# Kernel optimization log

Measured on AMD Instinct MI355X. Metric: run time of the kernel, lower is better.

## Reference

```python
import jax, jax.numpy as jnp
import numpy as np

N_NODES = 646  # fixed by nn.LayerNorm([646, 64])
LN_EPS = 1e-5


def gcn_conv(x, edge_index, W, b):
    """PyG GCNConv: out = D^-1/2 (A+I) D^-1/2 (x W) + b, scatter-add at target."""
    n = x.shape[0]
    h = x @ W  # [N, out_dim]
    loop = jnp.arange(n, dtype=edge_index.dtype)
    row = jnp.concatenate([edge_index[0], loop])  # source
    col = jnp.concatenate([edge_index[1], loop])  # target
    deg = jax.ops.segment_sum(jnp.ones_like(col, dtype=h.dtype), col, num_segments=n)
    dinv = jnp.where(deg > 0, jax.lax.rsqrt(deg), 0.0)
    norm = dinv[row] * dinv[col]  # [E+N]
    out = jax.ops.segment_sum(h[row] * norm[:, None], col, num_segments=n)
    return out + b


def setup_inputs() -> dict:
    key = jax.random.key(0)
    ks = jax.random.split(key, 8)
    F, H, L, E = 32768, 64, 128, 646 * 64
    x = jax.random.normal(ks[0], (N_NODES, F), dtype=jnp.float32)
    edge_index = jax.random.randint(ks[1], (2, E), 0, N_NODES, dtype=jnp.int64)
    s = 1.0 / np.sqrt(F)
    W1 = jax.random.normal(ks[2], (F, H), dtype=jnp.float32) * s
    b1 = jax.random.normal(ks[3], (H,), dtype=jnp.float32) * 0.01
    W2 = jax.random.normal(ks[4], (H, L), dtype=jnp.float32) * (1.0 / np.sqrt(H))
    b2 = jax.random.normal(ks[5], (L,), dtype=jnp.float32) * 0.01
    LPw = jax.random.normal(ks[6], (F, H), dtype=jnp.float32) * s
    LPb = jax.random.normal(ks[7], (H,), dtype=jnp.float32) * 0.01
    return {"x": x, "edge_index": edge_index, "W1": W1, "b1": b1,
            "W2": W2, "b2": b2, "LPw": LPw, "LPb": LPb}


def reference(x, edge_index, W1, b1, W2, b2, LPw, LPb):
    res = x @ LPw + LPb                       # Linear residual branch [N, 64]
    h = gcn_conv(x, edge_index, W1, b1)       # GCN1 [N, 64]
    h = res + h
    h = h * jax.nn.sigmoid(h)                 # SiLU
    # LayerNorm over BOTH dims [646, 64], no affine (elementwise_affine=False)
    mu = jnp.mean(h)
    var = jnp.mean(jnp.square(h - mu))
    h = (h - mu) * jax.lax.rsqrt(var + LN_EPS)
    out = gcn_conv(h, edge_index, W2, b2)     # GCN2 [N, num_label]
    return out
```

## Files before the change

kernel.cpp:

```cpp
#include <hip/hip_runtime.h>
#include <hip/hip_bf16.h>

#define NN 646
#define FF 32768
#define HH 64
#define LL 128
#define TOT (NN*HH)
#define OUTTOT (NN*LL)
#define WT_STRIDE (FF + 32)
#define KSPLIT 64
#define KSLICE (FF / KSPLIT)
#define BK 32
#define NSTEP (KSLICE / BK)
#define NMT 6
#define NGEMM (NMT * KSPLIT)

typedef float f32x4 __attribute__((ext_vector_type(4)));
typedef short short8 __attribute__((ext_vector_type(8)));

__device__ __forceinline__ unsigned short f2bf(float f) {
  __hip_bfloat16 h = __float2bfloat16(f);
  return __builtin_bit_cast(unsigned short, h);
}
__device__ __forceinline__ short8 pack8(float4 u, float4 v) {
  short8 r;
  r[0] = (short)f2bf(u.x); r[1] = (short)f2bf(u.y);
  r[2] = (short)f2bf(u.z); r[3] = (short)f2bf(u.w);
  r[4] = (short)f2bf(v.x); r[5] = (short)f2bf(v.y);
  r[6] = (short)f2bf(v.z); r[7] = (short)f2bf(v.w);
  return r;
}
__device__ __forceinline__ void gload16(const void* g, void* l) {
  __builtin_amdgcn_global_load_lds(
      (const __attribute__((address_space(1))) void*)g,
      (__attribute__((address_space(3))) void*)l, 16, 0, 0);
}
__device__ __forceinline__ bool probe_i64(const int* e32, int* orr) {
  if (threadIdx.x == 0) *orr = 0;
  __syncthreads();
  if (threadIdx.x < 256 && e32[2 * threadIdx.x + 1] != 0) atomicOr(orr, 1);
  __syncthreads();
  return *orr == 0;
}

__global__ __launch_bounds__(1024) void k_zero(int* __restrict__ cnt,
                                               float* __restrict__ stats) {
  int t = threadIdx.x;
  if (t < NN) cnt[t] = 0;
  if (t < 2) stats[t] = 0.f;
}

__global__ __launch_bounds__(256) void k_init(const float* __restrict__ W1,
                                              const float* __restrict__ LPw,
                                              unsigned short* __restrict__ wt,
                                              const int* __restrict__ e32, int E,
                                              int* __restrict__ cnt,
                                              const float* __restrict__ W2,
                                              float* __restrict__ cs) {
  if (blockIdx.x < 512) {
    __shared__ float t[64][129];
    int k0 = blockIdx.x * 64;
    for (int idx = threadIdx.x; idx < 64 * 128; idx += 256) {
      int kk = idx >> 7, n = idx & 127;
      float v = (n < 64) ? W1[(size_t)(k0 + kk) * 64 + n]
                         : LPw[(size_t)(k0 + kk) * 64 + (n - 64)];
      t[kk][n] = v;
    }
    __syncthreads();
    for (int idx = threadIdx.x; idx < 1024; idx += 256) {
      int n = idx >> 3;
      int kc = (idx & 7) * 8;
      short8 v;
#pragma unroll
      for (int u = 0; u < 8; ++u) v[u] = (short)f2bf(t[kc + u][n]);
      *reinterpret_cast<short8*>(&wt[(size_t)n * WT_STRIDE + k0 + kc]) = v;
    }
    return;
  }
  if (blockIdx.x == 576) {
    __shared__ float r2[2][128];
    int j = threadIdx.x & 127, h = threadIdx.x >> 7;
    float a = 0.f;
    for (int k = h * 32; k < h * 32 + 32; ++k) a += W2[k * LL + j];
    r2[h][j] = a;
    __syncthreads();
    if (h == 0) cs[j] = r2[0][j] + r2[1][j];
    return;
  }
  __shared__ int orr;
  bool i64 = probe_i64(e32, &orr);
  const int* cp = i64 ? (e32 + 2 * (size_t)E) : (e32 + E);
  int st = i64 ? 2 : 1;
  int wid = (blockIdx.x - 512) * 256 + threadIdx.x;
  for (int e = wid; e < E; e += 64 * 256)
    atomicAdd(&cnt[cp[(size_t)e * st]], 1);
}

__global__ __launch_bounds__(256, 3) void k_gemm(const float* __restrict__ x,
                                                 const unsigned short* __restrict__ wt,
                                                 float* __restrict__ partial,
                                                 const int* __restrict__ cnt, int E,
                                                 int* __restrict__ offsets,
                                                 float* __restrict__ dinv,
                                                 int* __restrict__ cursor) {
  __shared__ __align__(16) float As[2][128 * BK];
  __shared__ __align__(16) unsigned short Bs[2][128 * BK];

  int p = blockIdx.x;
  if (p == NGEMM) {
    __shared__ int wtot[4];
    int tid = threadIdx.x;
    int b = 3 * tid;
    int c0 = (b < NN) ? cnt[b] : 0;
    int c1 = (b + 1 < NN) ? cnt[b + 1] : 0;
    int c2 = (b + 2 < NN) ? cnt[b + 2] : 0;
    int s = c0 + c1 + c2;
    int lane = tid & 63, wv = tid >> 6;
    int run = s;
#pragma unroll
    for (int o = 1; o < 64; o <<= 1) { int v = __shfl_up(run, o); if (lane >= o) run += v; }
    if (lane == 63) wtot[wv] = run;
    __syncthreads();
    int wbase = 0;
    for (int i = 0; i < wv; ++i) wbase += wtot[i];
    int excl = wbase + run - s;
    if (b < NN)     { offsets[b]     = excl;           cursor[b]     = excl;           dinv[b]     = rsqrtf((float)(c0 + 1)); }
    if (b + 1 < NN) { offsets[b + 1] = excl + c0;      cursor[b + 1] = excl + c0;      dinv[b + 1] = rsqrtf((float)(c1 + 1)); }
    if (b + 2 < NN) { offsets[b + 2] = excl + c0 + c1; cursor[b + 2] = excl + c0 + c1; dinv[b + 2] = rsqrtf((float)(c2 + 1)); }
    if (tid == 0) offsets[NN] = E;
    return;
  }

  int xcd = p & 7, idx = p >> 3;
  int ks = xcd + 8 * (idx / NMT);
  int mt = idx % NMT;
  int tid = threadIdx.x;
  int w = tid >> 6, l = tid & 63;
  int lr = l & 15, g = l >> 4;
  int wr = w * 32;
  int ksbase = ks * KSLICE;

  f32x4 acc[2][8];
#pragma unroll
  for (int i = 0; i < 2; ++i)
#pragma unroll
    for (int j = 0; j < 8; ++j) acc[i][j] = (f32x4){0.f, 0.f, 0.f, 0.f};

  auto STAGE = [&](int buf, int step) {
    int kb = ksbase + step * BK;
#pragma unroll
    for (int j = 0; j < 4; ++j) {
      int pp = j * 256 + tid;
      int row = pp >> 3, cc = pp & 7;
      int c = cc ^ (row & 7);
      int rowg = mt * 128 + row; if (rowg > NN - 1) rowg = NN - 1;
      gload16(x + (size_t)rowg * FF + kb + c * 4, (char*)(&As[buf][0]) + pp * 16);
    }
#pragma unroll
    for (int j = 0; j < 2; ++j) {
      int pp = j * 256 + tid;
      int row = pp >> 2, cc = pp & 3;
      int c = cc ^ (row & 3);
      gload16(wt + (size_t)row * WT_STRIDE + kb + c * 8,
              (char*)(&Bs[buf][0]) + pp * 16);
    }
  };

  auto COMPUTE = [&](int buf) {
    const char* Ab = (const char*)(&As[buf][0]);
    const char* Bb = (const char*)(&Bs[buf][0]);
    short8 af0, af1;
    {
      int row = wr + lr, rm = row & 7;
      float4 lo = *(const float4*)(Ab + (row * 8 + ((g * 2) ^ rm)) * 16);
      float4 hi = *(const float4*)(Ab + (row * 8 + ((g * 2 + 1) ^ rm)) * 16);
      af0 = pack8(lo, hi);
    }
    {
      int row = wr + 16 + lr, rm = row & 7;
      float4 lo = *(const float4*)(Ab + (row * 8 + ((g * 2) ^ rm)) * 16);
      float4 hi = *(const float4*)(Ab + (row * 8 + ((g * 2 + 1) ^ rm)) * 16);
      af1 = pack8(lo, hi);
    }
#pragma unroll
    for (int nf = 0; nf < 8; ++nf) {
      int brow = nf * 16 + lr;
      short8 b = *(const short8*)(Bb + (brow * 4 + (g ^ (brow & 3))) * 16);
      acc[0][nf] = __builtin_amdgcn_mfma_f32_16x16x32_bf16(af0, b, acc[0][nf], 0, 0, 0);
      acc[1][nf] = __builtin_amdgcn_mfma_f32_16x16x32_bf16(af1, b, acc[1][nf], 0, 0, 0);
    }
  };

  STAGE(0, 0);
  STAGE(1, 1);
#pragma unroll
  for (int t = 0; t < NSTEP; ++t) {
    if (t + 1 < NSTEP) {
      asm volatile("s_waitcnt vmcnt(6)" ::: "memory");
    } else {
      asm volatile("s_waitcnt vmcnt(0)" ::: "memory");
    }
    __builtin_amdgcn_s_barrier();
    COMPUTE(t & 1);
    if (t + 2 < NSTEP) {
      __builtin_amdgcn_s_barrier();
      STAGE(t & 1, t + 2);
    }
  }

  float* pp = partial + (size_t)ks * OUTTOT;
#pragma unroll
  for (int mf = 0; mf < 2; ++mf) {
#pragma unroll
    for (int nf = 0; nf < 8; ++nf) {
#pragma unroll
      for (int j = 0; j < 4; ++j) {
        int m = mt * 128 + wr + mf * 16 + g * 4 + j;
        if (m < NN) pp[m * LL + nf * 16 + lr] = acc[mf][nf][j];
      }
    }
  }
}

__global__ __launch_bounds__(256) void k_redplace(const float* __restrict__ partial,
                                                  const float* __restrict__ LPb,
                                                  float* __restrict__ hcat,
                                                  const int* __restrict__ e32, int E,
                                                  int* __restrict__ cursor,
                                                  int* __restrict__ srcs) {
  if (blockIdx.x < 81) {
    int i4 = blockIdx.x * 256 + threadIdx.x;
    if (i4 * 4 >= OUTTOT) return;
    f32x4 s = {0.f, 0.f, 0.f, 0.f};
#pragma unroll 8
    for (int ks = 0; ks < KSPLIT; ++ks)
      s += *reinterpret_cast<const f32x4*>(partial + (size_t)ks * OUTTOT + i4 * 4);
    int n = (i4 * 4) & 127;
    if (n & 64) s += *reinterpret_cast<const f32x4*>(LPb + (n - 64));
    *reinterpret_cast<f32x4*>(hcat + i4 * 4) = s;
    return;
  }
  __shared__ int orr;
  bool i64 = probe_i64(e32, &orr);
  int e = (blockIdx.x - 81) * 256 + threadIdx.x;
  if (e >= E) return;
  const int* rp = e32;
  const int* cp = i64 ? (e32 + 2 * (size_t)E) : (e32 + E);
  int st = i64 ? 2 : 1;
  int r = rp[(size_t)e * st];
  int c = cp[(size_t)e * st];
  int pos = atomicAdd(&cursor[c], 1);
  srcs[pos] = r;
}

__global__ __launch_bounds__(256) void k_fuse1(const int* __restrict__ offs,
                                               const int* __restrict__ srcs,
                                               const float* __restrict__ dinv,
                                               const float* __restrict__ hcat,
                                               const float* __restrict__ b1,
                                               const float* __restrict__ W2,
                                               float* __restrict__ hwr,
                                               float* __restrict__ sdi,
                                               float* __restrict__ stats) {
  int c = blockIdx.x;
  int j = threadIdx.x & 63, qt = threadIdx.x >> 6;
  int o0 = offs[c], o1 = offs[c + 1];
  float acc = 0.f, sd = 0.f;
  for (int i = o0 + qt; i < o1; i += 4) {
    int r = srcs[i];
    float dr = dinv[r];
    acc += hcat[r * LL + j] * dr;
    sd += dr;
  }
  __shared__ float red[4][64];
  __shared__ float sdl[4];
  __shared__ float hnl[64];
  red[qt][j] = acc;
  if (j == 0) sdl[qt] = sd;
  __syncthreads();
  if (qt == 0) {
    float di = dinv[c];
    float gb = (red[0][j] + red[1][j] + red[2][j] + red[3][j]) * di;
    float t = hcat[c * LL + 64 + j] + b1[j] + gb + hcat[c * LL + j] * di * di;
    float s = t / (1.f + __expf(-t));
    hnl[j] = s;
    float sum = s, sq = s * s;
#pragma unroll
    for (int o = 32; o; o >>= 1) { sum += __shfl_down(sum, o); sq += __shfl_down(sq, o); }
    if (j == 0) {
      atomicAdd(&stats[0], sum);
      atomicAdd(&stats[1], sq);
      sdi[c] = sdl[0] + sdl[1] + sdl[2] + sdl[3] + di;
    }
  }
  __syncthreads();
  int j2 = threadIdx.x & 127, h = threadIdx.x >> 7;
  float a2 = 0.f;
#pragma unroll
  for (int k = h * 32; k < h * 32 + 32; ++k) a2 += hnl[k] * W2[k * LL + j2];
  __shared__ float r2[2][128];
  r2[h][j2] = a2;
  __syncthreads();
  if (h == 0) hwr[c * LL + j2] = (r2[0][j2] + r2[1][j2]) * dinv[c];
}

__global__ __launch_bounds__(256) void k_fuse2(const int* __restrict__ offs,
                                               const int* __restrict__ srcs,
                                               const float* __restrict__ dinv,
                                               const float* __restrict__ hwr,
                                               const float* __restrict__ b2,
                                               const float* __restrict__ cs,
                                               const float* __restrict__ sdi,
                                               const float* __restrict__ stats,
                                               float* __restrict__ out) {
  int c = blockIdx.x;
  int j = threadIdx.x & 127, hf = threadIdx.x >> 7;
  int o0 = offs[c], o1 = offs[c + 1];
  float acc = 0.f;
  for (int i = o0 + hf; i < o1; i += 2) acc += hwr[srcs[i] * LL + j];
  __shared__ float red[2][128];
  red[hf][j] = acc;
  __syncthreads();
  if (hf == 0) {
    float mu = stats[0] * (1.f / TOT);
    float var = stats[1] * (1.f / TOT) - mu * mu;
    float rs = rsqrtf(var + 1e-5f);
    float S = red[0][j] + red[1][j] + hwr[c * LL + j];
    out[c * LL + j] = b2[j] + dinv[c] * (rs * S - rs * mu * cs[j] * sdi[c]);
  }
}

extern "C" void kernel_launch(void* const* d_in, const int* in_sizes, int n_in,
                              void* d_out, int out_size, void* d_ws, size_t ws_size,
                              hipStream_t stream) {
  const float* x   = (const float*)d_in[0];
  const int*   e32 = (const int*)d_in[1];
  const float* W1  = (const float*)d_in[2];
  const float* b1  = (const float*)d_in[3];
  const float* W2  = (const float*)d_in[4];
  const float* b2  = (const float*)d_in[5];
  const float* LPw = (const float*)d_in[6];
  const float* LPb = (const float*)d_in[7];
  int E = in_sizes[1] / 2;
  float* out = (float*)d_out;

  char* ws = (char*)d_ws;
  size_t o_wt      = 0;
  size_t o_partial = 8396800;
  size_t o_hcat    = o_partial + (size_t)KSPLIT * OUTTOT * 4;
  size_t o_hwr     = o_hcat + 330752;
  size_t o_dinv    = o_hwr + 330752;
  size_t o_offs    = o_dinv + 2816;
  size_t o_cnt     = o_offs + 2816;
  size_t o_stat    = o_cnt + 2816;
  size_t o_cur     = o_stat + 256;
  size_t o_srcs    = o_cur + 2816;
  size_t o_cs      = o_srcs + 165376;
  size_t o_sdi     = o_cs + 512;

  unsigned short* wt = (unsigned short*)(ws + o_wt);
  float* partial = (float*)(ws + o_partial);
  float* hcat    = (float*)(ws + o_hcat);
  float* hwr     = (float*)(ws + o_hwr);
  float* dinv    = (float*)(ws + o_dinv);
  int*   offs    = (int*)(ws + o_offs);
  int*   cnt     = (int*)(ws + o_cnt);
  float* stats   = (float*)(ws + o_stat);
  int*   cursor  = (int*)(ws + o_cur);
  int*   srcs    = (int*)(ws + o_srcs);
  float* cs      = (float*)(ws + o_cs);
  float* sdi     = (float*)(ws + o_sdi);

  k_zero<<<1, 1024, 0, stream>>>(cnt, stats);
  k_init<<<577, 256, 0, stream>>>(W1, LPw, wt, e32, E, cnt, W2, cs);
  k_gemm<<<NGEMM + 1, 256, 0, stream>>>(x, wt, partial, cnt, E, offs, dinv, cursor);
  k_redplace<<<243, 256, 0, stream>>>(partial, LPb, hcat, e32, E, cursor, srcs);
  k_fuse1<<<NN, 256, 0, stream>>>(offs, srcs, dinv, hcat, b1, W2, hwr, sdi, stats);
  k_fuse2<<<NN, 256, 0, stream>>>(offs, srcs, dinv, hwr, b2, cs, sdi, stats, out);
}
```

Measured before the change: 94.20 us.

## Replace split-K partial buffer and reduction with atomic accumulation into hcat

The split-K GEMM now atomically adds its 64 partial tiles straight into hcat instead of writing a 64-slice partial buffer that a separate kernel summed. hcat is pre-filled with the LPb bias in a new pre-kernel that also zeroes the counters. The standalone edge-placement kernel keeps only the CSR scatter. This removes about 21 MB of partial writes and reads plus one reduction pass, at the cost of 64-way float atomic contention per output element and a summation order that is no longer deterministic.

```diff
diff --git a/kernel.cpp b/kernel.cpp
--- a/kernel.cpp
+++ b/kernel.cpp
@@ -43,10 +43,22 @@
   return *orr == 0;
 }
 
-__global__ __launch_bounds__(1024) void k_zero(int* __restrict__ cnt,
-                                               float* __restrict__ stats) {
+__global__ __launch_bounds__(256) void k_pre(const float* __restrict__ LPb,
+                                             float* __restrict__ hcat,
+                                             int* __restrict__ cnt,
+                                             float* __restrict__ stats) {
+  if (blockIdx.x < 81) {
+    int i4 = blockIdx.x * 256 + threadIdx.x;
+    if (i4 * 4 < OUTTOT) {
+      int n = (i4 * 4) & 127;
+      f32x4 v = {0.f, 0.f, 0.f, 0.f};
+      if (n & 64) v = *reinterpret_cast<const f32x4*>(LPb + (n - 64));
+      *reinterpret_cast<f32x4*>(hcat + i4 * 4) = v;
+    }
+    return;
+  }
   int t = threadIdx.x;
-  if (t < NN) cnt[t] = 0;
+  for (int i = t; i < 648; i += 256) cnt[i] = 0;
   if (t < 2) stats[t] = 0.f;
 }
 
@@ -98,7 +110,7 @@
 
 __global__ __launch_bounds__(256, 3) void k_gemm(const float* __restrict__ x,
                                                  const unsigned short* __restrict__ wt,
-                                                 float* __restrict__ partial,
+                                                 float* __restrict__ hcat,
                                                  const int* __restrict__ cnt, int E,
                                                  int* __restrict__ offsets,
                                                  float* __restrict__ dinv,
@@ -140,11 +152,9 @@
   int wr = w * 32;
   int ksbase = ks * KSLICE;
 
-  f32x4 acc[2][8];
-#pragma unroll
-  for (int i = 0; i < 2; ++i)
-#pragma unroll
-    for (int j = 0; j < 8; ++j) acc[i][j] = (f32x4){0.f, 0.f, 0.f, 0.f};
+  f32x4 z = {0.f, 0.f, 0.f, 0.f};
+  f32x4 a00 = z, a01 = z, a02 = z, a03 = z, a04 = z, a05 = z, a06 = z, a07 = z;
+  f32x4 a10 = z, a11 = z, a12 = z, a13 = z, a14 = z, a15 = z, a16 = z, a17 = z;
 
   auto STAGE = [&](int buf, int step) {
     int kb = ksbase + step * BK;
@@ -182,13 +192,16 @@
       float4 hi = *(const float4*)(Ab + (row * 8 + ((g * 2 + 1) ^ rm)) * 16);
       af1 = pack8(lo, hi);
     }
-#pragma unroll
-    for (int nf = 0; nf < 8; ++nf) {
-      int brow = nf * 16 + lr;
-      short8 b = *(const short8*)(Bb + (brow * 4 + (g ^ (brow & 3))) * 16);
-      acc[0][nf] = __builtin_amdgcn_mfma_f32_16x16x32_bf16(af0, b, acc[0][nf], 0, 0, 0);
-      acc[1][nf] = __builtin_amdgcn_mfma_f32_16x16x32_bf16(af1, b, acc[1][nf], 0, 0, 0);
-    }
+#define DO_NF(NF, A0, A1)                                                        \
+    {                                                                            \
+      int brow = NF * 16 + lr;                                                   \
+      short8 bv = *(const short8*)(Bb + (brow * 4 + (g ^ (brow & 3))) * 16);     \
+      A0 = __builtin_amdgcn_mfma_f32_16x16x32_bf16(af0, bv, A0, 0, 0, 0);        \
+      A1 = __builtin_amdgcn_mfma_f32_16x16x32_bf16(af1, bv, A1, 0, 0, 0);        \
+    }
+    DO_NF(0, a00, a10) DO_NF(1, a01, a11) DO_NF(2, a02, a12) DO_NF(3, a03, a13)
+    DO_NF(4, a04, a14) DO_NF(5, a05, a15) DO_NF(6, a06, a16) DO_NF(7, a07, a17)
+#undef DO_NF
   };
 
   STAGE(0, 0);
@@ -208,41 +221,27 @@
     }
   }
 
-  float* pp = partial + (size_t)ks * OUTTOT;
-#pragma unroll
-  for (int mf = 0; mf < 2; ++mf) {
-#pragma unroll
-    for (int nf = 0; nf < 8; ++nf) {
-#pragma unroll
-      for (int j = 0; j < 4; ++j) {
-        int m = mt * 128 + wr + mf * 16 + g * 4 + j;
-        if (m < NN) pp[m * LL + nf * 16 + lr] = acc[mf][nf][j];
-      }
-    }
-  }
-}
-
-__global__ __launch_bounds__(256) void k_redplace(const float* __restrict__ partial,
-                                                  const float* __restrict__ LPb,
-                                                  float* __restrict__ hcat,
-                                                  const int* __restrict__ e32, int E,
-                                                  int* __restrict__ cursor,
-                                                  int* __restrict__ srcs) {
-  if (blockIdx.x < 81) {
-    int i4 = blockIdx.x * 256 + threadIdx.x;
-    if (i4 * 4 >= OUTTOT) return;
-    f32x4 s = {0.f, 0.f, 0.f, 0.f};
-#pragma unroll 8
-    for (int ks = 0; ks < KSPLIT; ++ks)
-      s += *reinterpret_cast<const f32x4*>(partial + (size_t)ks * OUTTOT + i4 * 4);
-    int n = (i4 * 4) & 127;
-    if (n & 64) s += *reinterpret_cast<const f32x4*>(LPb + (n - 64));
-    *reinterpret_cast<f32x4*>(hcat + i4 * 4) = s;
-    return;
-  }
+#define EPI(MF, NF, ACC)                                                         \
+  {                                                                              \
+    _Pragma("unroll")                                                            \
+    for (int j = 0; j < 4; ++j) {                                                \
+      int m = mt * 128 + wr + MF * 16 + g * 4 + j;                               \
+      if (m < NN) atomicAdd(&hcat[m * LL + NF * 16 + lr], ACC[j]);               \
+    }                                                                            \
+  }
+  EPI(0, 0, a00) EPI(0, 1, a01) EPI(0, 2, a02) EPI(0, 3, a03)
+  EPI(0, 4, a04) EPI(0, 5, a05) EPI(0, 6, a06) EPI(0, 7, a07)
+  EPI(1, 0, a10) EPI(1, 1, a11) EPI(1, 2, a12) EPI(1, 3, a13)
+  EPI(1, 4, a14) EPI(1, 5, a15) EPI(1, 6, a16) EPI(1, 7, a17)
+#undef EPI
+}
+
+__global__ __launch_bounds__(256) void k_place(const int* __restrict__ e32, int E,
+                                               int* __restrict__ cursor,
+                                               int* __restrict__ srcs) {
   __shared__ int orr;
   bool i64 = probe_i64(e32, &orr);
-  int e = (blockIdx.x - 81) * 256 + threadIdx.x;
+  int e = blockIdx.x * 256 + threadIdx.x;
   if (e >= E) return;
   const int* rp = e32;
   const int* cp = i64 ? (e32 + 2 * (size_t)E) : (e32 + E);
@@ -345,36 +344,34 @@
   float* out = (float*)d_out;
 
   char* ws = (char*)d_ws;
-  size_t o_wt      = 0;
-  size_t o_partial = 8396800;
-  size_t o_hcat    = o_partial + (size_t)KSPLIT * OUTTOT * 4;
-  size_t o_hwr     = o_hcat + 330752;
-  size_t o_dinv    = o_hwr + 330752;
-  size_t o_offs    = o_dinv + 2816;
-  size_t o_cnt     = o_offs + 2816;
-  size_t o_stat    = o_cnt + 2816;
-  size_t o_cur     = o_stat + 256;
-  size_t o_srcs    = o_cur + 2816;
-  size_t o_cs      = o_srcs + 165376;
-  size_t o_sdi     = o_cs + 512;
+  size_t o_wt   = 0;
+  size_t o_hcat = 8396800;
+  size_t o_hwr  = o_hcat + 330752;
+  size_t o_dinv = o_hwr + 330752;
+  size_t o_offs = o_dinv + 2816;
+  size_t o_cnt  = o_offs + 2816;
+  size_t o_stat = o_cnt + 2816;
+  size_t o_cur  = o_stat + 256;
+  size_t o_srcs = o_cur + 2816;
+  size_t o_cs   = o_srcs + 165376;
+  size_t o_sdi  = o_cs + 512;
 
   unsigned short* wt = (unsigned short*)(ws + o_wt);
-  float* partial = (float*)(ws + o_partial);
-  float* hcat    = (float*)(ws + o_hcat);
-  float* hwr     = (float*)(ws + o_hwr);
-  float* dinv    = (float*)(ws + o_dinv);
-  int*   offs    = (int*)(ws + o_offs);
-  int*   cnt     = (int*)(ws + o_cnt);
-  float* stats   = (float*)(ws + o_stat);
-  int*   cursor  = (int*)(ws + o_cur);
-  int*   srcs    = (int*)(ws + o_srcs);
-  float* cs      = (float*)(ws + o_cs);
-  float* sdi     = (float*)(ws + o_sdi);
-
-  k_zero<<<1, 1024, 0, stream>>>(cnt, stats);
+  float* hcat   = (float*)(ws + o_hcat);
+  float* hwr    = (float*)(ws + o_hwr);
+  float* dinv   = (float*)(ws + o_dinv);
+  int*   offs   = (int*)(ws + o_offs);
+  int*   cnt    = (int*)(ws + o_cnt);
+  float* stats  = (float*)(ws + o_stat);
+  int*   cursor = (int*)(ws + o_cur);
+  int*   srcs   = (int*)(ws + o_srcs);
+  float* cs     = (float*)(ws + o_cs);
+  float* sdi    = (float*)(ws + o_sdi);
+
+  k_pre<<<82, 256, 0, stream>>>(LPb, hcat, cnt, stats);
   k_init<<<577, 256, 0, stream>>>(W1, LPw, wt, e32, E, cnt, W2, cs);
-  k_gemm<<<NGEMM + 1, 256, 0, stream>>>(x, wt, partial, cnt, E, offs, dinv, cursor);
-  k_redplace<<<243, 256, 0, stream>>>(partial, LPb, hcat, e32, E, cursor, srcs);
+  k_gemm<<<NGEMM + 1, 256, 0, stream>>>(x, wt, hcat, cnt, E, offs, dinv, cursor);
+  k_place<<<(E + 255) / 256, 256, 0, stream>>>(e32, E, cursor, srcs);
   k_fuse1<<<NN, 256, 0, stream>>>(offs, srcs, dinv, hcat, b1, W2, hwr, sdi, stats);
   k_fuse2<<<NN, 256, 0, stream>>>(offs, srcs, dinv, hwr, b2, cs, sdi, stats, out);
 }
```

Measured after the change: 109.3 us. 16.0% more time.

## Triple-buffer GEMM staging, per-block LDS histograms, drop zeroing kernel

Applied to the files above, without the earlier changes.

The GEMM main loop moves from double to triple LDS buffering. The next-next stage is issued before the current compute, so each step needs one barrier instead of two. This costs more shared memory and lowers the occupancy bound from 3 to 2 blocks per CU. Degree counting now uses per-block LDS histograms written to a partials array, which the scan block reduces. That removes the global atomics and the separate k_zero launch, with stats zeroed inside k_init. Accumulators are unrolled into named variables to keep them in registers.

```diff
diff --git a/kernel.cpp b/kernel.cpp
--- a/kernel.cpp
+++ b/kernel.cpp
@@ -43,20 +43,14 @@
   return *orr == 0;
 }
 
-__global__ __launch_bounds__(1024) void k_zero(int* __restrict__ cnt,
-                                               float* __restrict__ stats) {
-  int t = threadIdx.x;
-  if (t < NN) cnt[t] = 0;
-  if (t < 2) stats[t] = 0.f;
-}
-
 __global__ __launch_bounds__(256) void k_init(const float* __restrict__ W1,
                                               const float* __restrict__ LPw,
                                               unsigned short* __restrict__ wt,
                                               const int* __restrict__ e32, int E,
-                                              int* __restrict__ cnt,
+                                              int* __restrict__ cntp,
                                               const float* __restrict__ W2,
-                                              float* __restrict__ cs) {
+                                              float* __restrict__ cs,
+                                              float* __restrict__ stats) {
   if (blockIdx.x < 512) {
     __shared__ float t[64][129];
     int k0 = blockIdx.x * 64;
@@ -80,6 +74,7 @@
   if (blockIdx.x == 576) {
     __shared__ float r2[2][128];
     int j = threadIdx.x & 127, h = threadIdx.x >> 7;
+    if (threadIdx.x < 2) stats[threadIdx.x] = 0.f;
     float a = 0.f;
     for (int k = h * 32; k < h * 32 + 32; ++k) a += W2[k * LL + j];
     r2[h][j] = a;
@@ -87,33 +82,43 @@
     if (h == 0) cs[j] = r2[0][j] + r2[1][j];
     return;
   }
+  __shared__ int lcnt[648];
   __shared__ int orr;
+  int hb = blockIdx.x - 512;
+  for (int i = threadIdx.x; i < 648; i += 256) lcnt[i] = 0;
   bool i64 = probe_i64(e32, &orr);
   const int* cp = i64 ? (e32 + 2 * (size_t)E) : (e32 + E);
   int st = i64 ? 2 : 1;
-  int wid = (blockIdx.x - 512) * 256 + threadIdx.x;
-  for (int e = wid; e < E; e += 64 * 256)
-    atomicAdd(&cnt[cp[(size_t)e * st]], 1);
-}
-
-__global__ __launch_bounds__(256, 3) void k_gemm(const float* __restrict__ x,
+  for (int e = hb * 256 + threadIdx.x; e < E; e += 64 * 256)
+    atomicAdd(&lcnt[cp[(size_t)e * st]], 1);
+  __syncthreads();
+  for (int i = threadIdx.x; i < 648; i += 256) cntp[hb * 648 + i] = lcnt[i];
+}
+
+__global__ __launch_bounds__(256, 2) void k_gemm(const float* __restrict__ x,
                                                  const unsigned short* __restrict__ wt,
                                                  float* __restrict__ partial,
-                                                 const int* __restrict__ cnt, int E,
+                                                 const int* __restrict__ cntp, int E,
                                                  int* __restrict__ offsets,
                                                  float* __restrict__ dinv,
                                                  int* __restrict__ cursor) {
-  __shared__ __align__(16) float As[2][128 * BK];
-  __shared__ __align__(16) unsigned short Bs[2][128 * BK];
+  __shared__ __align__(16) float As[3][128 * BK];
+  __shared__ __align__(16) unsigned short Bs[3][128 * BK];
 
   int p = blockIdx.x;
   if (p == NGEMM) {
     __shared__ int wtot[4];
     int tid = threadIdx.x;
     int b = 3 * tid;
-    int c0 = (b < NN) ? cnt[b] : 0;
-    int c1 = (b + 1 < NN) ? cnt[b + 1] : 0;
-    int c2 = (b + 2 < NN) ? cnt[b + 2] : 0;
+    int c0 = 0, c1 = 0, c2 = 0;
+    if (b < NN) {
+#pragma unroll 8
+      for (int h = 0; h < 64; ++h) {
+        c0 += cntp[h * 648 + b];
+        c1 += (b + 1 < NN) ? cntp[h * 648 + b + 1] : 0;
+        c2 += (b + 2 < NN) ? cntp[h * 648 + b + 2] : 0;
+      }
+    }
     int s = c0 + c1 + c2;
     int lane = tid & 63, wv = tid >> 6;
     int run = s;
@@ -140,11 +145,9 @@
   int wr = w * 32;
   int ksbase = ks * KSLICE;
 
-  f32x4 acc[2][8];
-#pragma unroll
-  for (int i = 0; i < 2; ++i)
-#pragma unroll
-    for (int j = 0; j < 8; ++j) acc[i][j] = (f32x4){0.f, 0.f, 0.f, 0.f};
+  f32x4 z = {0.f, 0.f, 0.f, 0.f};
+  f32x4 a00 = z, a01 = z, a02 = z, a03 = z, a04 = z, a05 = z, a06 = z, a07 = z;
+  f32x4 a10 = z, a11 = z, a12 = z, a13 = z, a14 = z, a15 = z, a16 = z, a17 = z;
 
   auto STAGE = [&](int buf, int step) {
     int kb = ksbase + step * BK;
@@ -182,13 +185,16 @@
       float4 hi = *(const float4*)(Ab + (row * 8 + ((g * 2 + 1) ^ rm)) * 16);
       af1 = pack8(lo, hi);
     }
-#pragma unroll
-    for (int nf = 0; nf < 8; ++nf) {
-      int brow = nf * 16 + lr;
-      short8 b = *(const short8*)(Bb + (brow * 4 + (g ^ (brow & 3))) * 16);
-      acc[0][nf] = __builtin_amdgcn_mfma_f32_16x16x32_bf16(af0, b, acc[0][nf], 0, 0, 0);
-      acc[1][nf] = __builtin_amdgcn_mfma_f32_16x16x32_bf16(af1, b, acc[1][nf], 0, 0, 0);
-    }
+#define DO_NF(NF, A0, A1)                                                        \
+    {                                                                            \
+      int brow = NF * 16 + lr;                                                   \
+      short8 bv = *(const short8*)(Bb + (brow * 4 + (g ^ (brow & 3))) * 16);     \
+      A0 = __builtin_amdgcn_mfma_f32_16x16x32_bf16(af0, bv, A0, 0, 0, 0);        \
+      A1 = __builtin_amdgcn_mfma_f32_16x16x32_bf16(af1, bv, A1, 0, 0, 0);        \
+    }
+    DO_NF(0, a00, a10) DO_NF(1, a01, a11) DO_NF(2, a02, a12) DO_NF(3, a03, a13)
+    DO_NF(4, a04, a14) DO_NF(5, a05, a15) DO_NF(6, a06, a16) DO_NF(7, a07, a17)
+#undef DO_NF
   };
 
   STAGE(0, 0);
@@ -201,25 +207,24 @@
       asm volatile("s_waitcnt vmcnt(0)" ::: "memory");
     }
     __builtin_amdgcn_s_barrier();
-    COMPUTE(t & 1);
-    if (t + 2 < NSTEP) {
-      __builtin_amdgcn_s_barrier();
-      STAGE(t & 1, t + 2);
-    }
+    if (t + 2 < NSTEP) STAGE((t + 2) % 3, t + 2);
+    COMPUTE(t % 3);
   }
 
   float* pp = partial + (size_t)ks * OUTTOT;
-#pragma unroll
-  for (int mf = 0; mf < 2; ++mf) {
-#pragma unroll
-    for (int nf = 0; nf < 8; ++nf) {
-#pragma unroll
-      for (int j = 0; j < 4; ++j) {
-        int m = mt * 128 + wr + mf * 16 + g * 4 + j;
-        if (m < NN) pp[m * LL + nf * 16 + lr] = acc[mf][nf][j];
-      }
-    }
-  }
+#define EPI(MF, NF, ACC)                                                         \
+  {                                                                              \
+    _Pragma("unroll")                                                            \
+    for (int j = 0; j < 4; ++j) {                                                \
+      int m = mt * 128 + wr + MF * 16 + g * 4 + j;                               \
+      if (m < NN) pp[m * LL + NF * 16 + lr] = ACC[j];                            \
+    }                                                                            \
+  }
+  EPI(0, 0, a00) EPI(0, 1, a01) EPI(0, 2, a02) EPI(0, 3, a03)
+  EPI(0, 4, a04) EPI(0, 5, a05) EPI(0, 6, a06) EPI(0, 7, a07)
+  EPI(1, 0, a10) EPI(1, 1, a11) EPI(1, 2, a12) EPI(1, 3, a13)
+  EPI(1, 4, a14) EPI(1, 5, a15) EPI(1, 6, a16) EPI(1, 7, a17)
+#undef EPI
 }
 
 __global__ __launch_bounds__(256) void k_redplace(const float* __restrict__ partial,
@@ -351,8 +356,8 @@
   size_t o_hwr     = o_hcat + 330752;
   size_t o_dinv    = o_hwr + 330752;
   size_t o_offs    = o_dinv + 2816;
-  size_t o_cnt     = o_offs + 2816;
-  size_t o_stat    = o_cnt + 2816;
+  size_t o_cntp    = o_offs + 2816;
+  size_t o_stat    = o_cntp + 165888;
   size_t o_cur     = o_stat + 256;
   size_t o_srcs    = o_cur + 2816;
   size_t o_cs      = o_srcs + 165376;
@@ -364,16 +369,15 @@
   float* hwr     = (float*)(ws + o_hwr);
   float* dinv    = (float*)(ws + o_dinv);
   int*   offs    = (int*)(ws + o_offs);
-  int*   cnt     = (int*)(ws + o_cnt);
+  int*   cntp    = (int*)(ws + o_cntp);
   float* stats   = (float*)(ws + o_stat);
   int*   cursor  = (int*)(ws + o_cur);
   int*   srcs    = (int*)(ws + o_srcs);
   float* cs      = (float*)(ws + o_cs);
   float* sdi     = (float*)(ws + o_sdi);
 
-  k_zero<<<1, 1024, 0, stream>>>(cnt, stats);
-  k_init<<<577, 256, 0, stream>>>(W1, LPw, wt, e32, E, cnt, W2, cs);
-  k_gemm<<<NGEMM + 1, 256, 0, stream>>>(x, wt, partial, cnt, E, offs, dinv, cursor);
+  k_init<<<577, 256, 0, stream>>>(W1, LPw, wt, e32, E, cntp, W2, cs, stats);
+  k_gemm<<<NGEMM + 1, 256, 0, stream>>>(x, wt, partial, cntp, E, offs, dinv, cursor);
   k_redplace<<<243, 256, 0, stream>>>(partial, LPb, hcat, e32, E, cursor, srcs);
   k_fuse1<<<NN, 256, 0, stream>>>(offs, srcs, dinv, hcat, b1, W2, hwr, sdi, stats);
   k_fuse2<<<NN, 256, 0, stream>>>(offs, srcs, dinv, hwr, b2, cs, sdi, stats, out);
```

Result: faster. 80.76 us (-14.3%).
